# Optimization experiments

Measured on AMD Instinct MI355X. Metric: run time of the kernel, lower is better.

## Reference

```python
import jax, jax.numpy as jnp
import numpy as np
import math

B, S, D, H, DFF = 4, 2048, 1024, 16, 4096
DK = D // H
EPS = 1e-5

def setup_inputs() -> dict:
    key = jax.random.key(0)
    ks = jax.random.split(key, 16)
    s_d = 1.0 / math.sqrt(D)
    s_ff = 1.0 / math.sqrt(DFF)
    return {
        "x": jax.random.normal(ks[0], (B, S, D), jnp.float32),
        "wq": jax.random.uniform(ks[1], (D, D), jnp.float32, -s_d, s_d),
        "bq": jnp.zeros((D,), jnp.float32),
        "wk": jax.random.uniform(ks[2], (D, D), jnp.float32, -s_d, s_d),
        "bk": jnp.zeros((D,), jnp.float32),
        "wv": jax.random.uniform(ks[3], (D, D), jnp.float32, -s_d, s_d),
        "bv": jnp.zeros((D,), jnp.float32),
        "wo": jax.random.uniform(ks[4], (D, D), jnp.float32, -s_d, s_d),
        "bo": jnp.zeros((D,), jnp.float32),
        "w1": jax.random.uniform(ks[5], (DFF, D), jnp.float32, -s_d, s_d),
        "b1": jnp.zeros((DFF,), jnp.float32),
        "w2": jax.random.uniform(ks[6], (D, DFF), jnp.float32, -s_ff, s_ff),
        "b2": jnp.zeros((D,), jnp.float32),
        "ln1_g": jnp.ones((D,), jnp.float32),
        "ln1_b": jnp.zeros((D,), jnp.float32),
        "ln2_g": jnp.ones((D,), jnp.float32),
        "ln2_b": jnp.zeros((D,), jnp.float32),
    }

def _layernorm(x, g, b):
    mu = jnp.mean(x, axis=-1, keepdims=True)
    var = jnp.mean(jnp.square(x - mu), axis=-1, keepdims=True)
    return (x - mu) * jax.lax.rsqrt(var + EPS) * g + b

def reference(x, wq, bq, wk, bk, wv, bv, wo, bo, w1, b1, w2, b2, ln1_g, ln1_b, ln2_g, ln2_b):
    # Multi-head self-attention (dropout in eval mode -> identity).
    Q = (x @ wq.T + bq).reshape(B, S, H, DK).transpose(0, 2, 1, 3)  # (B,H,S,DK)
    K = (x @ wk.T + bk).reshape(B, S, H, DK).transpose(0, 2, 1, 3)
    V = (x @ wv.T + bv).reshape(B, S, H, DK).transpose(0, 2, 1, 3)
    scores = jnp.einsum('bhqd,bhkd->bhqk', Q, K) / math.sqrt(DK)  # (B,H,S,S)
    attn = jax.nn.softmax(scores, axis=-1)
    ctx = jnp.einsum('bhqk,bhkd->bhqd', attn, V)
    ctx = ctx.transpose(0, 2, 1, 3).reshape(B, S, D)
    attn_out = ctx @ wo.T + bo
    # SkipConnection: x + norm(sublayer)  (post-applied LayerNorm on sublayer output)
    x = x + _layernorm(attn_out, ln1_g, ln1_b)
    # FFN
    ff = jax.nn.relu(x @ w1.T + b1) @ w2.T + b2
    return x + _layernorm(ff, ln2_g, ln2_b)
```

## Files before the change

kernel.cpp:

```cpp
#include <hip/hip_runtime.h>
#include <hip/hip_bf16.h>
#include <stdint.h>


#define DI __device__ __forceinline__

typedef __attribute__((ext_vector_type(4))) float f32x4;
typedef __attribute__((ext_vector_type(16))) float f32x16;
typedef __attribute__((ext_vector_type(8))) short bf16x8;
typedef __attribute__((ext_vector_type(4))) short s16x4;

#define B_ 4
#define S_ 2048
#define D_ 1024
#define H_ 16
#define DK_ 64
#define DFF_ 4096
#define M_ 8192

DI float bf2f(short s) {
  union { unsigned u; float f; } v;
  v.u = ((unsigned)(unsigned short)s) << 16;
  return v.f;
}
DI short f2bf(float f) {
  union { float f; unsigned u; } v;
  v.f = f;
  unsigned r = v.u + 0x7FFFu + ((v.u >> 16) & 1u);
  return (short)(r >> 16);
}
DI unsigned pkbf(float lo, float hi) {
  unsigned r;
  asm("v_cvt_pk_bf16_f32 %0, %1, %2" : "=v"(r) : "v"(lo), "v"(hi));
  return r;
}
DI void plswap(unsigned& a, unsigned& b) {
  asm volatile("v_permlane32_swap_b32 %0, %1" : "+v"(a), "+v"(b));
}
DI float ex2(float x) {
  float r;
  asm("v_exp_f32 %0, %1" : "=v"(r) : "v"(x));
  return r;
}

__global__ __launch_bounds__(256) void cvt_kernel(const float* __restrict__ in,
                                                  short* __restrict__ out, int n) {
  long i = ((long)blockIdx.x * blockDim.x + threadIdx.x) * 8;
  if (i >= n) return;
  f32x4 a = *(const f32x4*)(in + i);
  f32x4 b = *(const f32x4*)(in + i + 4);
  bf16x8 r;
  r[0] = f2bf(a[0]); r[1] = f2bf(a[1]); r[2] = f2bf(a[2]); r[3] = f2bf(a[3]);
  r[4] = f2bf(b[0]); r[5] = f2bf(b[1]); r[6] = f2bf(b[2]); r[7] = f2bf(b[3]);
  *(bf16x8*)(out + i) = r;
}

DI void gl_lds16(const void* g, void* l) {
  __builtin_amdgcn_global_load_lds(
      (const __attribute__((address_space(1))) unsigned int*)g,
      (__attribute__((address_space(3))) unsigned int*)l, 16, 0, 0);
}

template <int BN, int MODE>
__global__ __launch_bounds__(512, 2)
void gemm_qs(const short* __restrict__ A, const short* __restrict__ Bm,
             const float* __restrict__ bias0, const float* __restrict__ bias1,
             const float* __restrict__ bias2, short* __restrict__ C,
             int M, int N, int K,
             short* __restrict__ Qo, short* __restrict__ Ko, short* __restrict__ Vo) {
  constexpr int NF = BN / 64;
  constexpr int WN = BN / 4;
  constexpr int ASLOT = 256 * 32;
  constexpr int BSLOT = BN * 32;

  __shared__ short As[4 * ASLOT];
  __shared__ short Bs[4 * BSLOT];

  const int t = threadIdx.x, w = t >> 6, l = t & 63;
  const int wm = w >> 2, wn = w & 3;
  const int lr = l & 15, lk = l >> 4;

  const int gx = gridDim.x;
  const int nwg = gx * gridDim.y;
  const int orig = blockIdx.y * gx + blockIdx.x;
  const int lin = (orig & 7) * (nwg >> 3) + (orig >> 3);
  const int row0 = (lin / gx) * 256;
  const int col0 = (lin % gx) * BN;

  const int NT = K >> 5;

  const int r0 = t >> 2, s0 = (((t & 3) ^ ((r0 >> 1) & 3)) << 3);
  const int r1 = r0 + 128, s1 = (((t & 3) ^ ((r1 >> 1) & 3)) << 3);
  const short* Asrc0 = A + (long)(row0 + r0) * K + s0;
  const short* Asrc1 = A + (long)(row0 + r1) * K + s1;
  const short* Bsrc0 = Bm + (long)(col0 + r0) * K + s0;
  const short* Bsrc1 = Bm + (long)(col0 + r1) * K + s1;
  const int d0 = t * 8, d1 = (t + 512) * 8;

  auto stageA = [&](int kt) {
    const int ko = kt << 5;
    short* Ab = As + (kt & 3) * ASLOT;
    gl_lds16(Asrc0 + ko, Ab + d0);
    gl_lds16(Asrc1 + ko, Ab + d1);
  };
  auto stageB = [&](int kt) {
    const int ko = kt << 5;
    short* Bb = Bs + (kt & 3) * BSLOT;
    gl_lds16(Bsrc0 + ko, Bb + d0);
    if constexpr (BN == 256) gl_lds16(Bsrc1 + ko, Bb + d1);
  };

  f32x4 acc[8][NF] = {};

  stageA(0); stageB(0);
  stageA(1); stageB(1);
  stageA(2); stageB(2);

  for (int kt = 0; kt < NT; ++kt) {
    if (kt + 2 < NT) {
      if constexpr (BN == 256) asm volatile("s_waitcnt vmcnt(8)" ::: "memory");
      else                     asm volatile("s_waitcnt vmcnt(6)" ::: "memory");
    } else if (kt + 1 < NT) {
      if constexpr (BN == 256) asm volatile("s_waitcnt vmcnt(4)" ::: "memory");
      else                     asm volatile("s_waitcnt vmcnt(3)" ::: "memory");
    } else {
      asm volatile("s_waitcnt vmcnt(0)" ::: "memory");
    }
    __builtin_amdgcn_s_barrier();

    const short* aw = As + (kt & 3) * ASLOT + wm * (128 * 32);
    const short* bw = Bs + (kt & 3) * BSLOT + wn * (WN * 32);

    bf16x8 afr[4], bfr[NF];
#pragma unroll
    for (int m = 0; m < 4; ++m) {
      const int rr = m * 16 + lr;
      afr[m] = *(const bf16x8*)(aw + rr * 32 + ((lk ^ ((rr >> 1) & 3)) << 3));
    }
#pragma unroll
    for (int n = 0; n < NF; ++n) {
      const int rr = n * 16 + lr;
      bfr[n] = *(const bf16x8*)(bw + rr * 32 + ((lk ^ ((rr >> 1) & 3)) << 3));
    }
    if (kt + 3 < NT) stageA(kt + 3);
    __builtin_amdgcn_s_barrier();
    asm volatile("s_waitcnt lgkmcnt(0)" ::: "memory");
    __builtin_amdgcn_sched_barrier(0);
    __builtin_amdgcn_s_setprio(1);
#pragma unroll
    for (int m = 0; m < 4; ++m)
#pragma unroll
      for (int n = 0; n < NF; ++n)
        acc[m][n] =
            __builtin_amdgcn_mfma_f32_16x16x32_bf16(afr[m], bfr[n], acc[m][n], 0, 0, 0);
    __builtin_amdgcn_s_setprio(0);

    bf16x8 af2[4];
#pragma unroll
    for (int m = 0; m < 4; ++m) {
      const int rr = 64 + m * 16 + lr;
      af2[m] = *(const bf16x8*)(aw + rr * 32 + ((lk ^ ((rr >> 1) & 3)) << 3));
    }
    if (kt + 3 < NT) stageB(kt + 3);
    __builtin_amdgcn_s_barrier();
    asm volatile("s_waitcnt lgkmcnt(0)" ::: "memory");
    __builtin_amdgcn_sched_barrier(0);
    __builtin_amdgcn_s_setprio(1);
#pragma unroll
    for (int m = 0; m < 4; ++m)
#pragma unroll
      for (int n = 0; n < NF; ++n)
        acc[4 + m][n] =
            __builtin_amdgcn_mfma_f32_16x16x32_bf16(af2[m], bfr[n], acc[4 + m][n], 0, 0, 0);
    __builtin_amdgcn_s_setprio(0);
  }

  if (MODE == 2) {
    const int which = col0 >> 10;
#pragma unroll
    for (int m = 0; m < 8; ++m) {
#pragma unroll
      for (int n = 0; n < NF; ++n) {
        const int r0e = row0 + wm * 128 + m * 16 + lk * 4;
        const int c = col0 + wn * WN + n * 16 + lr;
        const int cc = c & 1023;
        const int h = cc >> 6, dk = cc & 63;
        const int bb = r0e >> 11, s = r0e & 2047;
        if (which == 2) {
          const float bias = bias2[cc];
          s16x4 v4;
#pragma unroll
          for (int j = 0; j < 4; ++j) v4[j] = f2bf(acc[m][n][j] + bias);
          *(s16x4*)(Vo + ((long)((bb * H_ + h) * DK_ + dk)) * S_ + s) = v4;
        } else {
          const float bias = (which == 0 ? bias0[cc] : bias1[cc]);
          const float sc = (which == 0 ? 0.1803368801f : 1.0f);
          short* dst = (which == 0 ? Qo : Ko);
#pragma unroll
          for (int j = 0; j < 4; ++j)
            dst[(((long)(bb * H_ + h) * S_) + s + j) * DK_ + dk] =
                f2bf((acc[m][n][j] + bias) * sc);
        }
      }
    }
  } else {
#pragma unroll
    for (int m = 0; m < 8; ++m) {
#pragma unroll
      for (int n = 0; n < NF; ++n) {
#pragma unroll
        for (int j = 0; j < 4; ++j) {
          const int r = row0 + wm * 128 + m * 16 + lk * 4 + j;
          const int c = col0 + wn * WN + n * 16 + lr;
          float v = acc[m][n][j] + bias0[c];
          if (MODE == 1) v = fmaxf(v, 0.0f);
          C[(long)r * N + c] = f2bf(v);
        }
      }
    }
  }
}

__global__ __launch_bounds__(256, 4)
void attn_kernel(const short* __restrict__ Q, const short* __restrict__ K,
                 const short* __restrict__ Vt, short* __restrict__ ctx) {
  __shared__ short Ks[2 * 64 * 64];
  __shared__ short Vs[2 * 64 * 64];
  const int t = threadIdx.x, w = t >> 6, l = t & 63;
  const int q31 = l & 31, hi = l >> 5;
  const int bh = blockIdx.y;
  const int q0 = blockIdx.x * 128 + w * 32;
  const long base = (long)bh * S_ * DK_;

  bf16x8 qf[4];
  {
    const short* qp = Q + base + (long)(q0 + q31) * DK_ + hi * 8;
#pragma unroll
    for (int ks = 0; ks < 4; ++ks) qf[ks] = *(const bf16x8*)(qp + ks * 16);
  }

  f32x16 oa[2] = {};
  float mrun = -1e30f, lrun = 0.0f;

  const int srow = l >> 3;
  const int scol = ((l & 7) ^ srow) * 8;
  const int kr0 = w * 16 + srow, kr1 = w * 16 + 8 + srow;
  const int lw0 = w * 1024, lw1 = w * 1024 + 512;

  gl_lds16(K + base + (long)kr0 * DK_ + scol, &Ks[lw0]);
  gl_lds16(K + base + (long)kr1 * DK_ + scol, &Ks[lw1]);
  gl_lds16(Vt + base + (long)kr0 * S_ + scol, &Vs[lw0]);
  gl_lds16(Vt + base + (long)kr1 * S_ + scol, &Vs[lw1]);

  for (int tt = 0; tt < 32; ++tt) {
    asm volatile("s_waitcnt vmcnt(0)" ::: "memory");
    __builtin_amdgcn_s_barrier();
    if (tt + 1 < 32) {
      const int kb = ((tt + 1) & 1) * 4096;
      const int kvn = (tt + 1) * 64;
      gl_lds16(K + base + (long)(kvn + kr0) * DK_ + scol, &Ks[kb + lw0]);
      gl_lds16(K + base + (long)(kvn + kr1) * DK_ + scol, &Ks[kb + lw1]);
      gl_lds16(Vt + base + (long)kr0 * S_ + kvn + scol, &Vs[kb + lw0]);
      gl_lds16(Vt + base + (long)kr1 * S_ + kvn + scol, &Vs[kb + lw1]);
    }
    const int cb = (tt & 1) * 4096;

    f32x16 sacc[2] = {};
#pragma unroll
    for (int m = 0; m < 2; ++m) {
      const int row = m * 32 + q31;
      const int sw = row & 7;
#pragma unroll
      for (int ks = 0; ks < 4; ++ks) {
        bf16x8 kf = *(const bf16x8*)&Ks[cb + row * 64 + (((2 * ks + hi) ^ sw) << 3)];
        sacc[m] = __builtin_amdgcn_mfma_f32_32x32x16_bf16(kf, qf[ks], sacc[m], 0, 0, 0);
      }
    }

    float mx[8];
#pragma unroll
    for (int r = 0; r < 8; ++r)
      mx[r] = fmaxf(fmaxf(sacc[0][r], sacc[0][r + 8]),
                    fmaxf(sacc[1][r], sacc[1][r + 8]));
    mx[0] = fmaxf(mx[0], mx[4]); mx[1] = fmaxf(mx[1], mx[5]);
    mx[2] = fmaxf(mx[2], mx[6]); mx[3] = fmaxf(mx[3], mx[7]);
    float tm = fmaxf(fmaxf(mx[0], mx[1]), fmaxf(mx[2], mx[3]));
    tm = fmaxf(tm, __shfl_xor(tm, 32, 64));

    if (!__all(tm <= mrun + 8.0f)) {
      const float mnew = fmaxf(mrun, tm);
      const float fac = ex2(mrun - mnew);
      lrun *= fac;
#pragma unroll
      for (int m = 0; m < 2; ++m)
#pragma unroll
        for (int r = 0; r < 16; ++r) oa[m][r] *= fac;
      mrun = mnew;
    }

#pragma unroll
    for (int m = 0; m < 2; ++m)
#pragma unroll
      for (int r = 0; r < 16; ++r) sacc[m][r] = ex2(sacc[m][r] - mrun);

    float sm[8];
#pragma unroll
    for (int r = 0; r < 8; ++r)
      sm[r] = (sacc[0][r] + sacc[0][r + 8]) + (sacc[1][r] + sacc[1][r + 8]);
    sm[0] += sm[4]; sm[1] += sm[5]; sm[2] += sm[6]; sm[3] += sm[7];
    float ps = (sm[0] + sm[1]) + (sm[2] + sm[3]);
    ps += __shfl_xor(ps, 32, 64);
    lrun += ps;

    bf16x8 pf[4];
#pragma unroll
    for (int m = 0; m < 2; ++m)
#pragma unroll
      for (int sb = 0; sb < 2; ++sb) {
        unsigned p0 = pkbf(sacc[m][8 * sb + 0], sacc[m][8 * sb + 1]);
        unsigned p1 = pkbf(sacc[m][8 * sb + 2], sacc[m][8 * sb + 3]);
        unsigned p2 = pkbf(sacc[m][8 * sb + 4], sacc[m][8 * sb + 5]);
        unsigned p3 = pkbf(sacc[m][8 * sb + 6], sacc[m][8 * sb + 7]);
        plswap(p0, p2);
        plswap(p1, p3);
        union { unsigned u[4]; bf16x8 v; } fb;
        fb.u[0] = p0; fb.u[1] = p1; fb.u[2] = p2; fb.u[3] = p3;
        pf[2 * m + sb] = fb.v;
      }

#pragma unroll
    for (int mt = 0; mt < 2; ++mt) {
      const int row = mt * 32 + q31;
      const int sw = row & 7;
#pragma unroll
      for (int s = 0; s < 4; ++s) {
        bf16x8 vf = *(const bf16x8*)&Vs[cb + row * 64 + (((2 * s + hi) ^ sw) << 3)];
        oa[mt] = __builtin_amdgcn_mfma_f32_32x32x16_bf16(vf, pf[s], oa[mt], 0, 0, 0);
      }
    }
  }

  const int bb2 = bh >> 4, h = bh & 15;
  const float rl = 1.0f / lrun;
  short* crow = ctx + ((long)(bb2 * S_ + q0 + q31)) * D_ + h * 64 + 4 * hi;
#pragma unroll
  for (int mt = 0; mt < 2; ++mt)
#pragma unroll
    for (int g = 0; g < 4; ++g) {
      s16x4 v4;
#pragma unroll
      for (int i = 0; i < 4; ++i) v4[i] = f2bf(oa[mt][4 * g + i] * rl);
      *(s16x4*)(crow + mt * 32 + g * 8) = v4;
    }
}

template <int RES_BF16, int OUT_BF16>
__global__ __launch_bounds__(256)
void add_ln(const void* __restrict__ resv, const short* __restrict__ a,
            const float* __restrict__ gam, const float* __restrict__ bet,
            void* __restrict__ outv) {
  const int row = blockIdx.x, t = threadIdx.x;
  const int w = t >> 6, l = t & 63;
  const long roff = (long)row * D_;
  const int c = t * 4;
  s16x4 av = *(const s16x4*)(a + roff + c);
  float v0 = bf2f(av[0]), v1 = bf2f(av[1]), v2 = bf2f(av[2]), v3 = bf2f(av[3]);
  float s = v0 + v1 + v2 + v3;
#pragma unroll
  for (int mask = 1; mask < 64; mask <<= 1) s += __shfl_xor(s, mask, 64);
  __shared__ float r1[4], r2[4];
  if (l == 0) r1[w] = s;
  __syncthreads();
  float mu = (r1[0] + r1[1] + r1[2] + r1[3]) * (1.0f / D_);
  float d0 = v0 - mu, d1 = v1 - mu, d2 = v2 - mu, d3 = v3 - mu;
  float sq = d0 * d0 + d1 * d1 + d2 * d2 + d3 * d3;
#pragma unroll
  for (int mask = 1; mask < 64; mask <<= 1) sq += __shfl_xor(sq, mask, 64);
  if (l == 0) r2[w] = sq;
  __syncthreads();
  float var = (r2[0] + r2[1] + r2[2] + r2[3]) * (1.0f / D_);
  float rs = rsqrtf(var + 1e-5f);
  float res0, res1, res2, res3;
  if (RES_BF16) {
    s16x4 rv = *(const s16x4*)((const short*)resv + roff + c);
    res0 = bf2f(rv[0]); res1 = bf2f(rv[1]); res2 = bf2f(rv[2]); res3 = bf2f(rv[3]);
  } else {
    f32x4 rv = *(const f32x4*)((const float*)resv + roff + c);
    res0 = rv[0]; res1 = rv[1]; res2 = rv[2]; res3 = rv[3];
  }
  float o0 = res0 + d0 * rs * gam[c + 0] + bet[c + 0];
  float o1 = res1 + d1 * rs * gam[c + 1] + bet[c + 1];
  float o2 = res2 + d2 * rs * gam[c + 2] + bet[c + 2];
  float o3 = res3 + d3 * rs * gam[c + 3] + bet[c + 3];
  if (OUT_BF16) {
    s16x4 ov;
    ov[0] = f2bf(o0); ov[1] = f2bf(o1); ov[2] = f2bf(o2); ov[3] = f2bf(o3);
    *(s16x4*)((short*)outv + roff + c) = ov;
  } else {
    f32x4 ov;
    ov[0] = o0; ov[1] = o1; ov[2] = o2; ov[3] = o3;
    *(f32x4*)((float*)outv + roff + c) = ov;
  }
}

extern "C" void kernel_launch(void* const* d_in, const int* in_sizes, int n_in,
                              void* d_out, int out_size, void* d_ws, size_t ws_size,
                              hipStream_t stream) {
  (void)in_sizes; (void)n_in; (void)out_size; (void)ws_size;
  const float* x   = (const float*)d_in[0];
  const float* wq  = (const float*)d_in[1];
  const float* bq  = (const float*)d_in[2];
  const float* wk  = (const float*)d_in[3];
  const float* bk  = (const float*)d_in[4];
  const float* wv  = (const float*)d_in[5];
  const float* bv  = (const float*)d_in[6];
  const float* wo  = (const float*)d_in[7];
  const float* bo  = (const float*)d_in[8];
  const float* w1  = (const float*)d_in[9];
  const float* b1  = (const float*)d_in[10];
  const float* w2  = (const float*)d_in[11];
  const float* b2  = (const float*)d_in[12];
  const float* g1  = (const float*)d_in[13];
  const float* be1 = (const float*)d_in[14];
  const float* g2  = (const float*)d_in[15];
  const float* be2 = (const float*)d_in[16];

  char* ws = (char*)d_ws;
  const long MB = 1 << 20;
  short* xb    = (short*)(ws + 0 * MB);
  short* wqkvb = (short*)(ws + 16 * MB);
  short* wob   = (short*)(ws + 22 * MB);
  short* w1b   = (short*)(ws + 24 * MB);
  short* w2b   = (short*)(ws + 32 * MB);
  short* Qb    = (short*)(ws + 40 * MB);
  short* Kb    = (short*)(ws + 56 * MB);
  short* Vtb   = (short*)(ws + 72 * MB);
  short* ctxb  = (short*)(ws + 88 * MB);
  short* aout  = (short*)(ws + 40 * MB);
  short* x1b   = (short*)(ws + 56 * MB);
  short* hid   = (short*)(ws + 88 * MB);
  short* ffb   = (short*)(ws + 72 * MB);

  auto cvt = [&](const float* in, short* out, long n) {
    cvt_kernel<<<dim3((unsigned)((n / 8 + 255) / 256)), dim3(256), 0, stream>>>(in, out, (int)n);
  };
  cvt(x, xb, (long)M_ * D_);
  cvt(wq, wqkvb + 0L * D_ * D_, (long)D_ * D_);
  cvt(wk, wqkvb + 1L * D_ * D_, (long)D_ * D_);
  cvt(wv, wqkvb + 2L * D_ * D_, (long)D_ * D_);
  cvt(wo, wob, (long)D_ * D_);
  cvt(w1, w1b, (long)DFF_ * D_);
  cvt(w2, w2b, (long)D_ * DFF_);

  gemm_qs<256, 2><<<dim3(3072 / 256, M_ / 256), 512, 0, stream>>>(
      xb, wqkvb, bq, bk, bv, nullptr, M_, 3072, D_, Qb, Kb, Vtb);

  attn_kernel<<<dim3(S_ / 128, B_ * H_), 256, 0, stream>>>(Qb, Kb, Vtb, ctxb);

  gemm_qs<128, 0><<<dim3(D_ / 128, M_ / 256), 512, 0, stream>>>(
      ctxb, wob, bo, nullptr, nullptr, aout, M_, D_, D_, nullptr, nullptr, nullptr);

  add_ln<0, 1><<<dim3(M_), 256, 0, stream>>>(x, aout, g1, be1, x1b);

  gemm_qs<256, 1><<<dim3(DFF_ / 256, M_ / 256), 512, 0, stream>>>(
      x1b, w1b, b1, nullptr, nullptr, hid, M_, DFF_, D_, nullptr, nullptr, nullptr);
  gemm_qs<128, 0><<<dim3(D_ / 128, M_ / 256), 512, 0, stream>>>(
      hid, w2b, b2, nullptr, nullptr, ffb, M_, D_, DFF_, nullptr, nullptr, nullptr);

  add_ln<1, 0><<<dim3(M_), 256, 0, stream>>>(x1b, ffb, g2, be2, d_out);
}
```

Baseline: 419.5 us.

## Use 32x32 MFMA in GEMMs, triple-buffer attention K/V, remap blocks per XCD

The GEMM kernel switches from 16x16x32 to 32x32x16 bf16 MFMA tiles, with a matching fragment layout and rewritten epilogue indexing. Its workgroups are now remapped so each XCD handles a contiguous 2D region of the output, which should improve L2 reuse. The attention kernel moves from double to triple buffering of K/V in LDS with a two-tile prefetch and a partial vmcnt wait. It also remaps blocks so that each XCD processes whole heads. The extra LDS drops attention occupancy from 4 to 3 blocks, and the GEMM epilogue now issues more scalar stores.

```diff
diff --git a/kernel.cpp b/kernel.cpp
--- a/kernel.cpp
+++ b/kernel.cpp
@@ -63,12 +63,12 @@
 
 template <int BN, int MODE>
 __global__ __launch_bounds__(512, 2)
-void gemm_qs(const short* __restrict__ A, const short* __restrict__ Bm,
-             const float* __restrict__ bias0, const float* __restrict__ bias1,
-             const float* __restrict__ bias2, short* __restrict__ C,
-             int M, int N, int K,
-             short* __restrict__ Qo, short* __restrict__ Ko, short* __restrict__ Vo) {
-  constexpr int NF = BN / 64;
+void gemm_w32(const short* __restrict__ A, const short* __restrict__ Bm,
+              const float* __restrict__ bias0, const float* __restrict__ bias1,
+              const float* __restrict__ bias2, short* __restrict__ C,
+              int M, int N, int K,
+              short* __restrict__ Qo, short* __restrict__ Ko, short* __restrict__ Vo) {
+  constexpr int NB2 = BN / 128;
   constexpr int WN = BN / 4;
   constexpr int ASLOT = 256 * 32;
   constexpr int BSLOT = BN * 32;
@@ -78,23 +78,22 @@
 
   const int t = threadIdx.x, w = t >> 6, l = t & 63;
   const int wm = w >> 2, wn = w & 3;
-  const int lr = l & 15, lk = l >> 4;
-
-  const int gx = gridDim.x;
-  const int nwg = gx * gridDim.y;
+  const int l31 = l & 31, hi = l >> 5;
+
+  const int gx = gridDim.x, gy = gridDim.y;
   const int orig = blockIdx.y * gx + blockIdx.x;
-  const int lin = (orig & 7) * (nwg >> 3) + (orig >> 3);
-  const int row0 = (lin / gx) * 256;
-  const int col0 = (lin % gx) * BN;
+  const int xcd = orig & 7, k7 = orig >> 3;
+  const int rw = gx >> 1, rh = gy >> 2;
+  const int row0 = ((xcd >> 1) * rh + k7 / rw) * 256;
+  const int col0 = ((xcd & 1) * rw + k7 % rw) * BN;
 
   const int NT = K >> 5;
 
   const int r0 = t >> 2, s0 = (((t & 3) ^ ((r0 >> 1) & 3)) << 3);
-  const int r1 = r0 + 128, s1 = (((t & 3) ^ ((r1 >> 1) & 3)) << 3);
   const short* Asrc0 = A + (long)(row0 + r0) * K + s0;
-  const short* Asrc1 = A + (long)(row0 + r1) * K + s1;
+  const short* Asrc1 = A + (long)(row0 + 128 + r0) * K + s0;
   const short* Bsrc0 = Bm + (long)(col0 + r0) * K + s0;
-  const short* Bsrc1 = Bm + (long)(col0 + r1) * K + s1;
+  const short* Bsrc1 = Bm + (long)(col0 + 128 + r0) * K + s0;
   const int d0 = t * 8, d1 = (t + 512) * 8;
 
   auto stageA = [&](int kt) {
@@ -110,7 +109,7 @@
     if constexpr (BN == 256) gl_lds16(Bsrc1 + ko, Bb + d1);
   };
 
-  f32x4 acc[8][NF] = {};
+  f32x16 acc[4][NB2] = {};
 
   stageA(0); stageB(0);
   stageA(1); stageB(1);
@@ -131,16 +130,16 @@
     const short* aw = As + (kt & 3) * ASLOT + wm * (128 * 32);
     const short* bw = Bs + (kt & 3) * BSLOT + wn * (WN * 32);
 
-    bf16x8 afr[4], bfr[NF];
+    bf16x8 afr[4], bfr[NB2];
 #pragma unroll
     for (int m = 0; m < 4; ++m) {
-      const int rr = m * 16 + lr;
-      afr[m] = *(const bf16x8*)(aw + rr * 32 + ((lk ^ ((rr >> 1) & 3)) << 3));
-    }
-#pragma unroll
-    for (int n = 0; n < NF; ++n) {
-      const int rr = n * 16 + lr;
-      bfr[n] = *(const bf16x8*)(bw + rr * 32 + ((lk ^ ((rr >> 1) & 3)) << 3));
+      const int rr = m * 32 + l31;
+      afr[m] = *(const bf16x8*)(aw + rr * 32 + ((hi ^ ((rr >> 1) & 3)) << 3));
+    }
+#pragma unroll
+    for (int n = 0; n < NB2; ++n) {
+      const int rr = n * 32 + l31;
+      bfr[n] = *(const bf16x8*)(bw + rr * 32 + ((hi ^ ((rr >> 1) & 3)) << 3));
     }
     if (kt + 3 < NT) stageA(kt + 3);
     __builtin_amdgcn_s_barrier();
@@ -150,16 +149,21 @@
 #pragma unroll
     for (int m = 0; m < 4; ++m)
 #pragma unroll
-      for (int n = 0; n < NF; ++n)
+      for (int n = 0; n < NB2; ++n)
         acc[m][n] =
-            __builtin_amdgcn_mfma_f32_16x16x32_bf16(afr[m], bfr[n], acc[m][n], 0, 0, 0);
+            __builtin_amdgcn_mfma_f32_32x32x16_bf16(afr[m], bfr[n], acc[m][n], 0, 0, 0);
     __builtin_amdgcn_s_setprio(0);
 
-    bf16x8 af2[4];
+    bf16x8 af2[4], bf2[NB2];
 #pragma unroll
     for (int m = 0; m < 4; ++m) {
-      const int rr = 64 + m * 16 + lr;
-      af2[m] = *(const bf16x8*)(aw + rr * 32 + ((lk ^ ((rr >> 1) & 3)) << 3));
+      const int rr = m * 32 + l31;
+      af2[m] = *(const bf16x8*)(aw + rr * 32 + (((2 + hi) ^ ((rr >> 1) & 3)) << 3));
+    }
+#pragma unroll
+    for (int n = 0; n < NB2; ++n) {
+      const int rr = n * 32 + l31;
+      bf2[n] = *(const bf16x8*)(bw + rr * 32 + (((2 + hi) ^ ((rr >> 1) & 3)) << 3));
     }
     if (kt + 3 < NT) stageB(kt + 3);
     __builtin_amdgcn_s_barrier();
@@ -169,67 +173,74 @@
 #pragma unroll
     for (int m = 0; m < 4; ++m)
 #pragma unroll
-      for (int n = 0; n < NF; ++n)
-        acc[4 + m][n] =
-            __builtin_amdgcn_mfma_f32_16x16x32_bf16(af2[m], bfr[n], acc[4 + m][n], 0, 0, 0);
+      for (int n = 0; n < NB2; ++n)
+        acc[m][n] =
+            __builtin_amdgcn_mfma_f32_32x32x16_bf16(af2[m], bf2[n], acc[m][n], 0, 0, 0);
     __builtin_amdgcn_s_setprio(0);
   }
 
   if (MODE == 2) {
     const int which = col0 >> 10;
 #pragma unroll
-    for (int m = 0; m < 8; ++m) {
-#pragma unroll
-      for (int n = 0; n < NF; ++n) {
-        const int r0e = row0 + wm * 128 + m * 16 + lk * 4;
-        const int c = col0 + wn * WN + n * 16 + lr;
+    for (int m = 0; m < 4; ++m) {
+#pragma unroll
+      for (int n = 0; n < NB2; ++n) {
+        const int c = col0 + wn * WN + n * 32 + l31;
         const int cc = c & 1023;
         const int h = cc >> 6, dk = cc & 63;
-        const int bb = r0e >> 11, s = r0e & 2047;
-        if (which == 2) {
-          const float bias = bias2[cc];
-          s16x4 v4;
-#pragma unroll
-          for (int j = 0; j < 4; ++j) v4[j] = f2bf(acc[m][n][j] + bias);
-          *(s16x4*)(Vo + ((long)((bb * H_ + h) * DK_ + dk)) * S_ + s) = v4;
-        } else {
-          const float bias = (which == 0 ? bias0[cc] : bias1[cc]);
-          const float sc = (which == 0 ? 0.1803368801f : 1.0f);
-          short* dst = (which == 0 ? Qo : Ko);
-#pragma unroll
-          for (int j = 0; j < 4; ++j)
-            dst[(((long)(bb * H_ + h) * S_) + s + j) * DK_ + dk] =
-                f2bf((acc[m][n][j] + bias) * sc);
+#pragma unroll
+        for (int g = 0; g < 4; ++g) {
+          const int rg = row0 + wm * 128 + m * 32 + 8 * g + 4 * hi;
+          const int bb = rg >> 11, s = rg & 2047;
+          if (which == 2) {
+            const float bias = bias2[cc];
+            s16x4 v4;
+#pragma unroll
+            for (int j = 0; j < 4; ++j) v4[j] = f2bf(acc[m][n][4 * g + j] + bias);
+            *(s16x4*)(Vo + ((long)((bb * H_ + h) * DK_ + dk)) * S_ + s) = v4;
+          } else {
+            const float bias = (which == 0 ? bias0[cc] : bias1[cc]);
+            const float sc = (which == 0 ? 0.1803368801f : 1.0f);
+            short* dst = (which == 0 ? Qo : Ko);
+#pragma unroll
+            for (int j = 0; j < 4; ++j)
+              dst[(((long)(bb * H_ + h) * S_) + s + j) * DK_ + dk] =
+                  f2bf((acc[m][n][4 * g + j] + bias) * sc);
+          }
         }
       }
     }
   } else {
 #pragma unroll
-    for (int m = 0; m < 8; ++m) {
-#pragma unroll
-      for (int n = 0; n < NF; ++n) {
-#pragma unroll
-        for (int j = 0; j < 4; ++j) {
-          const int r = row0 + wm * 128 + m * 16 + lk * 4 + j;
-          const int c = col0 + wn * WN + n * 16 + lr;
-          float v = acc[m][n][j] + bias0[c];
+    for (int m = 0; m < 4; ++m) {
+#pragma unroll
+      for (int n = 0; n < NB2; ++n) {
+        const int c = col0 + wn * WN + n * 32 + l31;
+        const float bias = bias0[c];
+#pragma unroll
+        for (int r = 0; r < 16; ++r) {
+          const int row = row0 + wm * 128 + m * 32 + (r & 3) + 8 * (r >> 2) + 4 * hi;
+          float v = acc[m][n][r] + bias;
           if (MODE == 1) v = fmaxf(v, 0.0f);
-          C[(long)r * N + c] = f2bf(v);
+          C[(long)row * N + c] = f2bf(v);
         }
       }
     }
   }
 }
 
-__global__ __launch_bounds__(256, 4)
+__global__ __launch_bounds__(256, 3)
 void attn_kernel(const short* __restrict__ Q, const short* __restrict__ K,
                  const short* __restrict__ Vt, short* __restrict__ ctx) {
-  __shared__ short Ks[2 * 64 * 64];
-  __shared__ short Vs[2 * 64 * 64];
+  __shared__ short Ks[3 * 64 * 64];
+  __shared__ short Vs[3 * 64 * 64];
   const int t = threadIdx.x, w = t >> 6, l = t & 63;
   const int q31 = l & 31, hi = l >> 5;
-  const int bh = blockIdx.y;
-  const int q0 = blockIdx.x * 128 + w * 32;
+
+  const int orig = blockIdx.y * gridDim.x + blockIdx.x;
+  const int xcd = orig & 7, k7 = orig >> 3;
+  const int bh = xcd * 8 + (k7 >> 4);
+  const int q0 = (k7 & 15) * 128 + w * 32;
   const long base = (long)bh * S_ * DK_;
 
   bf16x8 qf[4];
@@ -247,23 +258,28 @@
   const int kr0 = w * 16 + srow, kr1 = w * 16 + 8 + srow;
   const int lw0 = w * 1024, lw1 = w * 1024 + 512;
 
-  gl_lds16(K + base + (long)kr0 * DK_ + scol, &Ks[lw0]);
-  gl_lds16(K + base + (long)kr1 * DK_ + scol, &Ks[lw1]);
-  gl_lds16(Vt + base + (long)kr0 * S_ + scol, &Vs[lw0]);
-  gl_lds16(Vt + base + (long)kr1 * S_ + scol, &Vs[lw1]);
-
+  auto stg = [&](int tile, int slot) {
+    const int kb = slot * 4096;
+    const int kvn = tile * 64;
+    gl_lds16(K + base + (long)(kvn + kr0) * DK_ + scol, &Ks[kb + lw0]);
+    gl_lds16(K + base + (long)(kvn + kr1) * DK_ + scol, &Ks[kb + lw1]);
+    gl_lds16(Vt + base + (long)kr0 * S_ + kvn + scol, &Vs[kb + lw0]);
+    gl_lds16(Vt + base + (long)kr1 * S_ + kvn + scol, &Vs[kb + lw1]);
+  };
+
+  stg(0, 0);
+  stg(1, 1);
+
+  int cs = 0;
   for (int tt = 0; tt < 32; ++tt) {
-    asm volatile("s_waitcnt vmcnt(0)" ::: "memory");
+    if (tt + 1 < 32) asm volatile("s_waitcnt vmcnt(4)" ::: "memory");
+    else             asm volatile("s_waitcnt vmcnt(0)" ::: "memory");
     __builtin_amdgcn_s_barrier();
-    if (tt + 1 < 32) {
-      const int kb = ((tt + 1) & 1) * 4096;
-      const int kvn = (tt + 1) * 64;
-      gl_lds16(K + base + (long)(kvn + kr0) * DK_ + scol, &Ks[kb + lw0]);
-      gl_lds16(K + base + (long)(kvn + kr1) * DK_ + scol, &Ks[kb + lw1]);
-      gl_lds16(Vt + base + (long)kr0 * S_ + kvn + scol, &Vs[kb + lw0]);
-      gl_lds16(Vt + base + (long)kr1 * S_ + kvn + scol, &Vs[kb + lw1]);
-    }
-    const int cb = (tt & 1) * 4096;
+    if (tt + 2 < 32) {
+      int ss = cs + 2; if (ss >= 3) ss -= 3;
+      stg(tt + 2, ss);
+    }
+    const int cb = cs * 4096;
 
     f32x16 sacc[2] = {};
 #pragma unroll
@@ -338,6 +354,7 @@
         oa[mt] = __builtin_amdgcn_mfma_f32_32x32x16_bf16(vf, pf[s], oa[mt], 0, 0, 0);
       }
     }
+    cs = (cs == 2) ? 0 : cs + 1;
   }
 
   const int bb2 = bh >> 4, h = bh & 15;
@@ -452,19 +469,19 @@
   cvt(w1, w1b, (long)DFF_ * D_);
   cvt(w2, w2b, (long)D_ * DFF_);
 
-  gemm_qs<256, 2><<<dim3(3072 / 256, M_ / 256), 512, 0, stream>>>(
+  gemm_w32<256, 2><<<dim3(3072 / 256, M_ / 256), 512, 0, stream>>>(
       xb, wqkvb, bq, bk, bv, nullptr, M_, 3072, D_, Qb, Kb, Vtb);
 
   attn_kernel<<<dim3(S_ / 128, B_ * H_), 256, 0, stream>>>(Qb, Kb, Vtb, ctxb);
 
-  gemm_qs<128, 0><<<dim3(D_ / 128, M_ / 256), 512, 0, stream>>>(
+  gemm_w32<128, 0><<<dim3(D_ / 128, M_ / 256), 512, 0, stream>>>(
       ctxb, wob, bo, nullptr, nullptr, aout, M_, D_, D_, nullptr, nullptr, nullptr);
 
   add_ln<0, 1><<<dim3(M_), 256, 0, stream>>>(x, aout, g1, be1, x1b);
 
-  gemm_qs<256, 1><<<dim3(DFF_ / 256, M_ / 256), 512, 0, stream>>>(
+  gemm_w32<256, 1><<<dim3(DFF_ / 256, M_ / 256), 512, 0, stream>>>(
       x1b, w1b, b1, nullptr, nullptr, hid, M_, DFF_, D_, nullptr, nullptr, nullptr);
-  gemm_qs<128, 0><<<dim3(D_ / 128, M_ / 256), 512, 0, stream>>>(
+  gemm_w32<128, 0><<<dim3(D_ / 128, M_ / 256), 512, 0, stream>>>(
       hid, w2b, b2, nullptr, nullptr, ffb, M_, D_, DFF_, nullptr, nullptr, nullptr);
 
   add_ln<1, 0><<<dim3(M_), 256, 0, stream>>>(x1b, ffb, g2, be2, d_out);
```

Result: no change. 420.1 us (+0.1%).

## Rewrite GEMM as 8-wave double-buffered K64 pipeline with XCD-aware tile mapping

Applied to the files above, without the earlier changes.

Replaces the GEMM's K=32 four-slot ring with a K=64 double-buffered scheme. A and B halves are staged in interleaved quarters between MFMA phases, occupancy is set to one block per CU, and a new XCD-aware block-to-tile remap groups neighbouring tiles on the same XCD. The attention kernel also remaps blocks so each XCD handles contiguous heads, and it uses v_max3 for the row-max reduction. This trades deeper prefetch for a finer-grained overlap of loads with compute, aiming for better L2 locality, but it risks lower latency hiding at one block per CU.

```diff
diff --git a/kernel.cpp b/kernel.cpp
--- a/kernel.cpp
+++ b/kernel.cpp
@@ -40,6 +40,11 @@
 DI float ex2(float x) {
   float r;
   asm("v_exp_f32 %0, %1" : "=v"(r) : "v"(x));
+  return r;
+}
+DI float max3(float a, float b, float c) {
+  float r;
+  asm("v_max3_f32 %0, %1, %2, %3" : "=v"(r) : "v"(a), "v"(b), "v"(c));
   return r;
 }
 
@@ -61,118 +66,211 @@
       (__attribute__((address_space(3))) unsigned int*)l, 16, 0, 0);
 }
 
+#define VMCNT(N) asm volatile("s_waitcnt vmcnt(" #N ")" ::: "memory")
+#define LGKM0                                          \
+  asm volatile("s_waitcnt lgkmcnt(0)" ::: "memory");   \
+  __builtin_amdgcn_sched_barrier(0)
+
 template <int BN, int MODE>
-__global__ __launch_bounds__(512, 2)
-void gemm_qs(const short* __restrict__ A, const short* __restrict__ Bm,
-             const float* __restrict__ bias0, const float* __restrict__ bias1,
-             const float* __restrict__ bias2, short* __restrict__ C,
-             int M, int N, int K,
-             short* __restrict__ Qo, short* __restrict__ Ko, short* __restrict__ Vo) {
+__global__ __launch_bounds__(512, 1)
+void gemm8w(const short* __restrict__ A, const short* __restrict__ Bm,
+            const float* __restrict__ bias0, const float* __restrict__ bias1,
+            const float* __restrict__ bias2, short* __restrict__ C,
+            int M, int N, int K,
+            short* __restrict__ Qo, short* __restrict__ Ko, short* __restrict__ Vo) {
   constexpr int NF = BN / 64;
   constexpr int WN = BN / 4;
-  constexpr int ASLOT = 256 * 32;
-  constexpr int BSLOT = BN * 32;
-
-  __shared__ short As[4 * ASLOT];
-  __shared__ short Bs[4 * BSLOT];
+  constexpr int BH = BN / 128;
+
+  __shared__ short As[2 * 2 * 8192];
+  __shared__ short Bs[2 * BH * 8192];
 
   const int t = threadIdx.x, w = t >> 6, l = t & 63;
   const int wm = w >> 2, wn = w & 3;
   const int lr = l & 15, lk = l >> 4;
 
-  const int gx = gridDim.x;
-  const int nwg = gx * gridDim.y;
+  const int gx = gridDim.x, gy = gridDim.y;
   const int orig = blockIdx.y * gx + blockIdx.x;
-  const int lin = (orig & 7) * (nwg >> 3) + (orig >> 3);
-  const int row0 = (lin / gx) * 256;
-  const int col0 = (lin % gx) * BN;
-
-  const int NT = K >> 5;
-
-  const int r0 = t >> 2, s0 = (((t & 3) ^ ((r0 >> 1) & 3)) << 3);
-  const int r1 = r0 + 128, s1 = (((t & 3) ^ ((r1 >> 1) & 3)) << 3);
-  const short* Asrc0 = A + (long)(row0 + r0) * K + s0;
-  const short* Asrc1 = A + (long)(row0 + r1) * K + s1;
-  const short* Bsrc0 = Bm + (long)(col0 + r0) * K + s0;
-  const short* Bsrc1 = Bm + (long)(col0 + r1) * K + s1;
-  const int d0 = t * 8, d1 = (t + 512) * 8;
-
-  auto stageA = [&](int kt) {
-    const int ko = kt << 5;
-    short* Ab = As + (kt & 3) * ASLOT;
-    gl_lds16(Asrc0 + ko, Ab + d0);
-    gl_lds16(Asrc1 + ko, Ab + d1);
+  const int xcd = orig & 7, k7 = orig >> 3;
+  const int rw = gx >> 1, rh = gy >> 2;
+  const int row0 = ((xcd >> 1) * rh + k7 / rw) * 256;
+  const int col0 = ((xcd & 1) * rw + k7 % rw) * BN;
+
+  const int NT = K >> 6;
+
+  const int rl0 = t >> 3;
+  const int csw = (((t & 7) ^ ((t >> 3) & 7)) << 3);
+  const short* Abase = A + (long)row0 * K;
+  const short* Bbase = Bm + (long)col0 * K;
+
+  auto stA = [&](int kt, int h) {
+    short* dst = As + (((kt & 1) * 2 + h) << 13);
+    const short* s = Abase + (long)(h * 128 + rl0) * K + (kt << 6) + csw;
+    gl_lds16(s, dst + t * 8);
+    gl_lds16(s + (long)64 * K, dst + (t + 512) * 8);
   };
-  auto stageB = [&](int kt) {
-    const int ko = kt << 5;
-    short* Bb = Bs + (kt & 3) * BSLOT;
-    gl_lds16(Bsrc0 + ko, Bb + d0);
-    if constexpr (BN == 256) gl_lds16(Bsrc1 + ko, Bb + d1);
+  auto stB = [&](int kt, int h) {
+    short* dst = Bs + (((kt & 1) * BH + h) << 13);
+    const short* s = Bbase + (long)(h * 128 + rl0) * K + (kt << 6) + csw;
+    gl_lds16(s, dst + t * 8);
+    gl_lds16(s + (long)64 * K, dst + (t + 512) * 8);
   };
 
   f32x4 acc[8][NF] = {};
-
-  stageA(0); stageB(0);
-  stageA(1); stageB(1);
-  stageA(2); stageB(2);
+  bf16x8 afr[4][2], af2[4][2], bfr[2][2], bf2[2][2], bf3[2][2];
+
+  if (BH == 2) { stA(0, 0); stB(0, 0); stB(0, 1); stA(0, 1); }
+  else         { stA(0, 0); stB(0, 0); stA(0, 1); }
 
   for (int kt = 0; kt < NT; ++kt) {
-    if (kt + 2 < NT) {
-      if constexpr (BN == 256) asm volatile("s_waitcnt vmcnt(8)" ::: "memory");
-      else                     asm volatile("s_waitcnt vmcnt(6)" ::: "memory");
-    } else if (kt + 1 < NT) {
-      if constexpr (BN == 256) asm volatile("s_waitcnt vmcnt(4)" ::: "memory");
-      else                     asm volatile("s_waitcnt vmcnt(3)" ::: "memory");
+    const bool more = (kt + 1 < NT);
+    const short* aw = As + (((kt & 1) * 2 + wm) << 13);
+
+    if (BH == 2) {
+      const short* bw = Bs + (((kt & 1) * 2 + (wn >> 1)) << 13);
+      const int bro = (wn & 1) * 64;
+      VMCNT(4);
+      __builtin_amdgcn_s_barrier();
+      if (more) stA(kt + 1, 0);
+#pragma unroll
+      for (int m = 0; m < 4; ++m) {
+        const int r = m * 16 + lr;
+#pragma unroll
+        for (int kk = 0; kk < 2; ++kk)
+          afr[m][kk] = *(const bf16x8*)(aw + r * 64 + (((lk + 4 * kk) ^ (r & 7)) << 3));
+      }
+#pragma unroll
+      for (int n = 0; n < 2; ++n) {
+        const int r = bro + n * 16 + lr;
+#pragma unroll
+        for (int kk = 0; kk < 2; ++kk)
+          bfr[n][kk] = *(const bf16x8*)(bw + r * 64 + (((lk + 4 * kk) ^ (r & 7)) << 3));
+      }
+      LGKM0;
+      __builtin_amdgcn_s_setprio(1);
+#pragma unroll
+      for (int m = 0; m < 4; ++m)
+#pragma unroll
+        for (int n = 0; n < 2; ++n)
+#pragma unroll
+          for (int kk = 0; kk < 2; ++kk)
+            acc[m][n] = __builtin_amdgcn_mfma_f32_16x16x32_bf16(
+                afr[m][kk], bfr[n][kk], acc[m][n], 0, 0, 0);
+      __builtin_amdgcn_s_setprio(0);
+      if (more) { VMCNT(4); } else { VMCNT(2); }
+      __builtin_amdgcn_s_barrier();
+      if (more) stB(kt + 1, 0);
+#pragma unroll
+      for (int n = 0; n < 2; ++n) {
+        const int r = bro + 32 + n * 16 + lr;
+#pragma unroll
+        for (int kk = 0; kk < 2; ++kk)
+          bf2[n][kk] = *(const bf16x8*)(bw + r * 64 + (((lk + 4 * kk) ^ (r & 7)) << 3));
+      }
+      LGKM0;
+      __builtin_amdgcn_s_setprio(1);
+#pragma unroll
+      for (int m = 0; m < 4; ++m)
+#pragma unroll
+        for (int n = 0; n < 2; ++n)
+#pragma unroll
+          for (int kk = 0; kk < 2; ++kk)
+            acc[m][2 + n] = __builtin_amdgcn_mfma_f32_16x16x32_bf16(
+                afr[m][kk], bf2[n][kk], acc[m][2 + n], 0, 0, 0);
+      __builtin_amdgcn_s_setprio(0);
+      if (more) { VMCNT(4); } else { VMCNT(0); }
+      __builtin_amdgcn_s_barrier();
+      if (more) stB(kt + 1, 1);
+#pragma unroll
+      for (int m = 0; m < 4; ++m) {
+        const int r = 64 + m * 16 + lr;
+#pragma unroll
+        for (int kk = 0; kk < 2; ++kk)
+          af2[m][kk] = *(const bf16x8*)(aw + r * 64 + (((lk + 4 * kk) ^ (r & 7)) << 3));
+      }
+      LGKM0;
+      __builtin_amdgcn_s_setprio(1);
+#pragma unroll
+      for (int m = 0; m < 4; ++m)
+#pragma unroll
+        for (int n = 0; n < 2; ++n)
+#pragma unroll
+          for (int kk = 0; kk < 2; ++kk)
+            acc[4 + m][2 + n] = __builtin_amdgcn_mfma_f32_16x16x32_bf16(
+                af2[m][kk], bf2[n][kk], acc[4 + m][2 + n], 0, 0, 0);
+      __builtin_amdgcn_s_setprio(0);
+      if (more) stA(kt + 1, 1);
+#pragma unroll
+      for (int n = 0; n < 2; ++n) {
+        const int r = bro + n * 16 + lr;
+#pragma unroll
+        for (int kk = 0; kk < 2; ++kk)
+          bf3[n][kk] = *(const bf16x8*)(bw + r * 64 + (((lk + 4 * kk) ^ (r & 7)) << 3));
+      }
+      LGKM0;
+      __builtin_amdgcn_s_setprio(1);
+#pragma unroll
+      for (int m = 0; m < 4; ++m)
+#pragma unroll
+        for (int n = 0; n < 2; ++n)
+#pragma unroll
+          for (int kk = 0; kk < 2; ++kk)
+            acc[4 + m][n] = __builtin_amdgcn_mfma_f32_16x16x32_bf16(
+                af2[m][kk], bf3[n][kk], acc[4 + m][n], 0, 0, 0);
+      __builtin_amdgcn_s_setprio(0);
     } else {
-      asm volatile("s_waitcnt vmcnt(0)" ::: "memory");
-    }
-    __builtin_amdgcn_s_barrier();
-
-    const short* aw = As + (kt & 3) * ASLOT + wm * (128 * 32);
-    const short* bw = Bs + (kt & 3) * BSLOT + wn * (WN * 32);
-
-    bf16x8 afr[4], bfr[NF];
-#pragma unroll
-    for (int m = 0; m < 4; ++m) {
-      const int rr = m * 16 + lr;
-      afr[m] = *(const bf16x8*)(aw + rr * 32 + ((lk ^ ((rr >> 1) & 3)) << 3));
-    }
-#pragma unroll
-    for (int n = 0; n < NF; ++n) {
-      const int rr = n * 16 + lr;
-      bfr[n] = *(const bf16x8*)(bw + rr * 32 + ((lk ^ ((rr >> 1) & 3)) << 3));
-    }
-    if (kt + 3 < NT) stageA(kt + 3);
-    __builtin_amdgcn_s_barrier();
-    asm volatile("s_waitcnt lgkmcnt(0)" ::: "memory");
-    __builtin_amdgcn_sched_barrier(0);
-    __builtin_amdgcn_s_setprio(1);
-#pragma unroll
-    for (int m = 0; m < 4; ++m)
-#pragma unroll
-      for (int n = 0; n < NF; ++n)
-        acc[m][n] =
-            __builtin_amdgcn_mfma_f32_16x16x32_bf16(afr[m], bfr[n], acc[m][n], 0, 0, 0);
-    __builtin_amdgcn_s_setprio(0);
-
-    bf16x8 af2[4];
-#pragma unroll
-    for (int m = 0; m < 4; ++m) {
-      const int rr = 64 + m * 16 + lr;
-      af2[m] = *(const bf16x8*)(aw + rr * 32 + ((lk ^ ((rr >> 1) & 3)) << 3));
-    }
-    if (kt + 3 < NT) stageB(kt + 3);
-    __builtin_amdgcn_s_barrier();
-    asm volatile("s_waitcnt lgkmcnt(0)" ::: "memory");
-    __builtin_amdgcn_sched_barrier(0);
-    __builtin_amdgcn_s_setprio(1);
-#pragma unroll
-    for (int m = 0; m < 4; ++m)
-#pragma unroll
-      for (int n = 0; n < NF; ++n)
-        acc[4 + m][n] =
-            __builtin_amdgcn_mfma_f32_16x16x32_bf16(af2[m], bfr[n], acc[4 + m][n], 0, 0, 0);
-    __builtin_amdgcn_s_setprio(0);
+      const short* bw = Bs + (((kt & 1) * BH) << 13);
+      const int bro = wn * 32;
+      VMCNT(2);
+      __builtin_amdgcn_s_barrier();
+      if (more) { stA(kt + 1, 0); stB(kt + 1, 0); }
+#pragma unroll
+      for (int m = 0; m < 4; ++m) {
+        const int r = m * 16 + lr;
+#pragma unroll
+        for (int kk = 0; kk < 2; ++kk)
+          afr[m][kk] = *(const bf16x8*)(aw + r * 64 + (((lk + 4 * kk) ^ (r & 7)) << 3));
+      }
+#pragma unroll
+      for (int n = 0; n < 2; ++n) {
+        const int r = bro + n * 16 + lr;
+#pragma unroll
+        for (int kk = 0; kk < 2; ++kk)
+          bfr[n][kk] = *(const bf16x8*)(bw + r * 64 + (((lk + 4 * kk) ^ (r & 7)) << 3));
+      }
+      LGKM0;
+      __builtin_amdgcn_s_setprio(1);
+#pragma unroll
+      for (int m = 0; m < 4; ++m)
+#pragma unroll
+        for (int n = 0; n < 2; ++n)
+#pragma unroll
+          for (int kk = 0; kk < 2; ++kk)
+            acc[m][n] = __builtin_amdgcn_mfma_f32_16x16x32_bf16(
+                afr[m][kk], bfr[n][kk], acc[m][n], 0, 0, 0);
+      __builtin_amdgcn_s_setprio(0);
+      if (more) { VMCNT(4); } else { VMCNT(0); }
+      __builtin_amdgcn_s_barrier();
+      if (more) stA(kt + 1, 1);
+#pragma unroll
+      for (int m = 0; m < 4; ++m) {
+        const int r = 64 + m * 16 + lr;
+#pragma unroll
+        for (int kk = 0; kk < 2; ++kk)
+          af2[m][kk] = *(const bf16x8*)(aw + r * 64 + (((lk + 4 * kk) ^ (r & 7)) << 3));
+      }
+      LGKM0;
+      __builtin_amdgcn_s_setprio(1);
+#pragma unroll
+      for (int m = 0; m < 4; ++m)
+#pragma unroll
+        for (int n = 0; n < 2; ++n)
+#pragma unroll
+          for (int kk = 0; kk < 2; ++kk)
+            acc[4 + m][n] = __builtin_amdgcn_mfma_f32_16x16x32_bf16(
+                af2[m][kk], bfr[n][kk], acc[4 + m][n], 0, 0, 0);
+      __builtin_amdgcn_s_setprio(0);
+    }
   }
 
   if (MODE == 2) {
@@ -228,8 +326,11 @@
   __shared__ short Vs[2 * 64 * 64];
   const int t = threadIdx.x, w = t >> 6, l = t & 63;
   const int q31 = l & 31, hi = l >> 5;
-  const int bh = blockIdx.y;
-  const int q0 = blockIdx.x * 128 + w * 32;
+
+  const int orig = blockIdx.y * gridDim.x + blockIdx.x;
+  const int xcd = orig & 7, k7 = orig >> 3;
+  const int bh = xcd * 8 + (k7 >> 4);
+  const int q0 = (k7 & 15) * 128 + w * 32;
   const long base = (long)bh * S_ * DK_;
 
   bf16x8 qf[4];
@@ -247,22 +348,21 @@
   const int kr0 = w * 16 + srow, kr1 = w * 16 + 8 + srow;
   const int lw0 = w * 1024, lw1 = w * 1024 + 512;
 
-  gl_lds16(K + base + (long)kr0 * DK_ + scol, &Ks[lw0]);
-  gl_lds16(K + base + (long)kr1 * DK_ + scol, &Ks[lw1]);
-  gl_lds16(Vt + base + (long)kr0 * S_ + scol, &Vs[lw0]);
-  gl_lds16(Vt + base + (long)kr1 * S_ + scol, &Vs[lw1]);
+  auto stg = [&](int tile, int slot) {
+    const int kb = slot * 4096;
+    const int kvn = tile * 64;
+    gl_lds16(K + base + (long)(kvn + kr0) * DK_ + scol, &Ks[kb + lw0]);
+    gl_lds16(K + base + (long)(kvn + kr1) * DK_ + scol, &Ks[kb + lw1]);
+    gl_lds16(Vt + base + (long)kr0 * S_ + kvn + scol, &Vs[kb + lw0]);
+    gl_lds16(Vt + base + (long)kr1 * S_ + kvn + scol, &Vs[kb + lw1]);
+  };
+
+  stg(0, 0);
 
   for (int tt = 0; tt < 32; ++tt) {
-    asm volatile("s_waitcnt vmcnt(0)" ::: "memory");
+    VMCNT(0);
     __builtin_amdgcn_s_barrier();
-    if (tt + 1 < 32) {
-      const int kb = ((tt + 1) & 1) * 4096;
-      const int kvn = (tt + 1) * 64;
-      gl_lds16(K + base + (long)(kvn + kr0) * DK_ + scol, &Ks[kb + lw0]);
-      gl_lds16(K + base + (long)(kvn + kr1) * DK_ + scol, &Ks[kb + lw1]);
-      gl_lds16(Vt + base + (long)kr0 * S_ + kvn + scol, &Vs[kb + lw0]);
-      gl_lds16(Vt + base + (long)kr1 * S_ + kvn + scol, &Vs[kb + lw1]);
-    }
+    if (tt + 1 < 32) stg(tt + 1, (tt + 1) & 1);
     const int cb = (tt & 1) * 4096;
 
     f32x16 sacc[2] = {};
@@ -280,11 +380,10 @@
     float mx[8];
 #pragma unroll
     for (int r = 0; r < 8; ++r)
-      mx[r] = fmaxf(fmaxf(sacc[0][r], sacc[0][r + 8]),
-                    fmaxf(sacc[1][r], sacc[1][r + 8]));
-    mx[0] = fmaxf(mx[0], mx[4]); mx[1] = fmaxf(mx[1], mx[5]);
-    mx[2] = fmaxf(mx[2], mx[6]); mx[3] = fmaxf(mx[3], mx[7]);
-    float tm = fmaxf(fmaxf(mx[0], mx[1]), fmaxf(mx[2], mx[3]));
+      mx[r] = fmaxf(max3(sacc[0][r], sacc[0][r + 8], sacc[1][r]), sacc[1][r + 8]);
+    float ma = max3(mx[0], mx[1], mx[2]);
+    float mb = max3(mx[3], mx[4], mx[5]);
+    float tm = fmaxf(max3(mx[6], mx[7], ma), mb);
     tm = fmaxf(tm, __shfl_xor(tm, 32, 64));
 
     if (!__all(tm <= mrun + 8.0f)) {
@@ -452,19 +551,19 @@
   cvt(w1, w1b, (long)DFF_ * D_);
   cvt(w2, w2b, (long)D_ * DFF_);
 
-  gemm_qs<256, 2><<<dim3(3072 / 256, M_ / 256), 512, 0, stream>>>(
+  gemm8w<256, 2><<<dim3(3072 / 256, M_ / 256), 512, 0, stream>>>(
       xb, wqkvb, bq, bk, bv, nullptr, M_, 3072, D_, Qb, Kb, Vtb);
 
   attn_kernel<<<dim3(S_ / 128, B_ * H_), 256, 0, stream>>>(Qb, Kb, Vtb, ctxb);
 
-  gemm_qs<128, 0><<<dim3(D_ / 128, M_ / 256), 512, 0, stream>>>(
+  gemm8w<128, 0><<<dim3(D_ / 128, M_ / 256), 512, 0, stream>>>(
       ctxb, wob, bo, nullptr, nullptr, aout, M_, D_, D_, nullptr, nullptr, nullptr);
 
   add_ln<0, 1><<<dim3(M_), 256, 0, stream>>>(x, aout, g1, be1, x1b);
 
-  gemm_qs<256, 1><<<dim3(DFF_ / 256, M_ / 256), 512, 0, stream>>>(
+  gemm8w<256, 1><<<dim3(DFF_ / 256, M_ / 256), 512, 0, stream>>>(
       x1b, w1b, b1, nullptr, nullptr, hid, M_, DFF_, D_, nullptr, nullptr, nullptr);
-  gemm_qs<128, 0><<<dim3(D_ / 128, M_ / 256), 512, 0, stream>>>(
+  gemm8w<128, 0><<<dim3(D_ / 128, M_ / 256), 512, 0, stream>>>(
       hid, w2b, b2, nullptr, nullptr, ffb, M_, D_, DFF_, nullptr, nullptr, nullptr);
 
   add_ln<1, 0><<<dim3(M_), 256, 0, stream>>>(x1b, ffb, g2, be2, d_out);
```

Result: slower. 469.4 us (+11.9%).
